# Kernel optimization log

Measured on AMD Instinct MI355X. Metric: run time of the kernel, lower is better.

The kernel has to match this reference:

```python
import jax, jax.numpy as jnp
import numpy as np

# PointPillars canonical grid / channels / batch
NY, NX, C, B = 496, 432, 64, 2
N_PER = 12000  # non-empty pillars per batch element


def setup_inputs() -> dict:
    key = jax.random.key(0)
    voxel_features = jax.random.normal(key, (B * N_PER, C), dtype=jnp.float32)
    # Build coords [N,4] = (batch_id, z, y, x) with UNIQUE grid cells per batch
    # (matches PointPillars: each pillar occupies a distinct (y,x) cell).
    rng = np.random.default_rng(0)
    lins = np.concatenate([rng.choice(NY * NX, size=N_PER, replace=False) for _ in range(B)])
    ys = lins // NX
    xs = lins % NX
    bids = np.repeat(np.arange(B), N_PER)
    coords = np.stack([bids, np.zeros_like(bids), ys, xs], axis=1).astype(np.int64)
    return {"voxel_features": voxel_features, "coords": jnp.asarray(coords)}


def reference(voxel_features, coords):
    # voxel_features: [N, C] float; coords: [N, 4] int (batch, z, y, x)
    lin = coords[:, 2] * NX + coords[:, 3]          # [N] linear cell index
    bid = coords[:, 0]                              # [N] batch id
    canvas = jnp.zeros((B, C, NY * NX), dtype=voxel_features.dtype)
    # One fused scatter: writes voxel_features[n, :] to canvas[bid[n], :, lin[n]]
    canvas = canvas.at[bid, :, lin].set(voxel_features)
    return canvas.reshape(B, C, NY, NX)
```

## Files before the change

### kernel.cpp

```cpp
#include <hip/hip_runtime.h>


#define NYc 496
#define NXc 432
#define Cc  64
#define Bc  2
#define NPIX (NYc * NXc)
#define NQ   (NPIX / 4)


__global__ void pps_scatter_idx(const int* __restrict__ coords,
                                int* __restrict__ idx, int n_pts) {
    int n = blockIdx.x * blockDim.x + threadIdx.x;
    if (n >= n_pts) return;
    int bid = coords[n * 4 + 0];
    int y   = coords[n * 4 + 2];
    int x   = coords[n * 4 + 3];
    idx[bid * NPIX + y * NXc + x] = n;
}

__global__ void pps_gather(const float* __restrict__ feat,
                           const int* __restrict__ idx,
                           float* __restrict__ out) {
    int q = blockIdx.x * blockDim.x + threadIdx.x;
    if (q >= NQ) return;
    int plane = blockIdx.y;
    int b = plane >> 6;
    int c = plane & 63;

    const int4 pid4 = *reinterpret_cast<const int4*>(idx + (size_t)b * NPIX + (size_t)q * 4);
    float4 v;
    v.x = (pid4.x >= 0) ? feat[(size_t)pid4.x * Cc + c] : 0.0f;
    v.y = (pid4.y >= 0) ? feat[(size_t)pid4.y * Cc + c] : 0.0f;
    v.z = (pid4.z >= 0) ? feat[(size_t)pid4.z * Cc + c] : 0.0f;
    v.w = (pid4.w >= 0) ? feat[(size_t)pid4.w * Cc + c] : 0.0f;
    *reinterpret_cast<float4*>(out + (size_t)plane * NPIX + (size_t)q * 4) = v;
}


__global__ void pps_scatter_feat(const float* __restrict__ feat,
                                 const int* __restrict__ coords,
                                 float* __restrict__ out, int n_pts) {
    int t = blockIdx.x * blockDim.x + threadIdx.x;
    int n = t >> 6;
    int c = t & 63;
    if (n >= n_pts) return;
    int bid = coords[n * 4 + 0];
    int y   = coords[n * 4 + 2];
    int x   = coords[n * 4 + 3];
    out[((size_t)(bid * Cc + c)) * NPIX + (size_t)y * NXc + x] = feat[(size_t)n * Cc + c];
}

extern "C" void kernel_launch(void* const* d_in, const int* in_sizes, int n_in,
                              void* d_out, int out_size, void* d_ws, size_t ws_size,
                              hipStream_t stream) {
    const float* feat   = (const float*)d_in[0];
    const int*   coords = (const int*)d_in[1];
    float*       out    = (float*)d_out;
    int n_pts = in_sizes[1] / 4;

    size_t idx_bytes = (size_t)Bc * NPIX * sizeof(int);

    if (ws_size >= idx_bytes) {
        int* idx = (int*)d_ws;
        hipMemsetAsync(idx, 0xFF, idx_bytes, stream);
        pps_scatter_idx<<<dim3((n_pts + 255) / 256), dim3(256), 0, stream>>>(coords, idx, n_pts);
        dim3 grid((NQ + 255) / 256, Bc * Cc);
        pps_gather<<<grid, dim3(256), 0, stream>>>(feat, idx, out);
    } else {
        hipMemsetAsync(out, 0, (size_t)out_size * sizeof(float), stream);
        long long total = (long long)n_pts * Cc;
        pps_scatter_feat<<<dim3((unsigned)((total + 255) / 256)), dim3(256), 0, stream>>>(
            feat, coords, out, n_pts);
    }
}
```

Baseline: 35.95 us.

## Gather four channels per thread with vector loads and nontemporal stores

The gather kernel now makes each thread handle four consecutive channels for four pixels. It loads one 16-byte float4 of features per pillar and transposes the 4x4 block in registers. This cuts index reloads by a factor of four and turns scalar feature loads into vector loads, and the output writes use nontemporal stores to avoid polluting the cache. The hipMemsetAsync on the index buffer is replaced by a small init kernel that fills it with -1. In exchange, the grid gets four times fewer blocks in y and each thread holds more registers.

```diff
diff --git a/kernel.cpp b/kernel.cpp
--- a/kernel.cpp
+++ b/kernel.cpp
@@ -7,7 +7,18 @@
 #define Bc  2
 #define NPIX (NYc * NXc)
 #define NQ   (NPIX / 4)
+#define NIDX4 ((Bc * NPIX) / 4)
 
+typedef float f32x4 __attribute__((ext_vector_type(4)));
+typedef int   i32x4 __attribute__((ext_vector_type(4)));
+
+__global__ void pps_init_idx(i32x4* __restrict__ idx4) {
+    int i = blockIdx.x * blockDim.x + threadIdx.x;
+    if (i < NIDX4) {
+        i32x4 m1 = {-1, -1, -1, -1};
+        idx4[i] = m1;
+    }
+}
 
 __global__ void pps_scatter_idx(const int* __restrict__ coords,
                                 int* __restrict__ idx, int n_pts) {
@@ -19,22 +30,34 @@
     idx[bid * NPIX + y * NXc + x] = n;
 }
 
-__global__ void pps_gather(const float* __restrict__ feat,
-                           const int* __restrict__ idx,
-                           float* __restrict__ out) {
+__global__ void pps_gather4(const float* __restrict__ feat,
+                            const int* __restrict__ idx,
+                            float* __restrict__ out) {
     int q = blockIdx.x * blockDim.x + threadIdx.x;
     if (q >= NQ) return;
-    int plane = blockIdx.y;
-    int b = plane >> 6;
-    int c = plane & 63;
+    int g  = blockIdx.y;
+    int b  = g >> 4;
+    int c0 = (g & 15) << 2;
 
-    const int4 pid4 = *reinterpret_cast<const int4*>(idx + (size_t)b * NPIX + (size_t)q * 4);
-    float4 v;
-    v.x = (pid4.x >= 0) ? feat[(size_t)pid4.x * Cc + c] : 0.0f;
-    v.y = (pid4.y >= 0) ? feat[(size_t)pid4.y * Cc + c] : 0.0f;
-    v.z = (pid4.z >= 0) ? feat[(size_t)pid4.z * Cc + c] : 0.0f;
-    v.w = (pid4.w >= 0) ? feat[(size_t)pid4.w * Cc + c] : 0.0f;
-    *reinterpret_cast<float4*>(out + (size_t)plane * NPIX + (size_t)q * 4) = v;
+    const i32x4 pid4 = *reinterpret_cast<const i32x4*>(idx + (size_t)b * NPIX + (size_t)q * 4);
+
+    f32x4 zero = {0.f, 0.f, 0.f, 0.f};
+    f32x4 f0 = zero, f1 = zero, f2 = zero, f3 = zero;
+    if (pid4.x >= 0) f0 = *reinterpret_cast<const f32x4*>(feat + (size_t)pid4.x * Cc + c0);
+    if (pid4.y >= 0) f1 = *reinterpret_cast<const f32x4*>(feat + (size_t)pid4.y * Cc + c0);
+    if (pid4.z >= 0) f2 = *reinterpret_cast<const f32x4*>(feat + (size_t)pid4.z * Cc + c0);
+    if (pid4.w >= 0) f3 = *reinterpret_cast<const f32x4*>(feat + (size_t)pid4.w * Cc + c0);
+
+    f32x4 o0 = {f0.x, f1.x, f2.x, f3.x};
+    f32x4 o1 = {f0.y, f1.y, f2.y, f3.y};
+    f32x4 o2 = {f0.z, f1.z, f2.z, f3.z};
+    f32x4 o3 = {f0.w, f1.w, f2.w, f3.w};
+
+    size_t base = ((size_t)(b * Cc + c0)) * NPIX + (size_t)q * 4;
+    __builtin_nontemporal_store(o0, reinterpret_cast<f32x4*>(out + base));
+    __builtin_nontemporal_store(o1, reinterpret_cast<f32x4*>(out + base + (size_t)NPIX));
+    __builtin_nontemporal_store(o2, reinterpret_cast<f32x4*>(out + base + (size_t)2 * NPIX));
+    __builtin_nontemporal_store(o3, reinterpret_cast<f32x4*>(out + base + (size_t)3 * NPIX));
 }
 
 
@@ -63,12 +86,12 @@
 
     if (ws_size >= idx_bytes) {
         int* idx = (int*)d_ws;
-        hipMemsetAsync(idx, 0xFF, idx_bytes, stream);
+        pps_init_idx<<<dim3((NIDX4 + 255) / 256), dim3(256), 0, stream>>>((i32x4*)idx);
         pps_scatter_idx<<<dim3((n_pts + 255) / 256), dim3(256), 0, stream>>>(coords, idx, n_pts);
-        dim3 grid((NQ + 255) / 256, Bc * Cc);
-        pps_gather<<<grid, dim3(256), 0, stream>>>(feat, idx, out);
+        dim3 grid((NQ + 255) / 256, (Bc * Cc) / 4);
+        pps_gather4<<<grid, dim3(256), 0, stream>>>(feat, idx, out);
     } else {
-        hipMemsetAsync(out, 0, (size_t)out_size * sizeof(float), stream);
+        (void)hipMemsetAsync(out, 0, (size_t)out_size * sizeof(float), stream);
         long long total = (long long)n_pts * Cc;
         pps_scatter_feat<<<dim3((unsigned)((total + 255) / 256)), dim3(256), 0, stream>>>(
             feat, coords, out, n_pts);
```

After: 33.66 us. 6.4% less time.
